# Kernel optimization log

Measured on AMD Instinct MI355X. Metric: run time of the kernel, lower is better.

## Reference

```python
import jax, jax.numpy as jnp
import numpy as np

B = 16384
WIDE_DIM = 256          # 32 wide features * dim 8
DEEP_DIM = 1024         # 64 deep features * embedding_dim 16
SHARED = [2048, 1024, 512]
DOMAIN = [512, 256]
NUM_DOMAINS = 8


def setup_inputs() -> dict:
    key = jax.random.key(0)
    ks = jax.random.split(key, 20)
    s = 0.01  # embedding_init_var-style small init
    inp = {
        "wide_features": jax.random.normal(ks[0], (B, WIDE_DIM), jnp.float32),
        "deep_features": jax.random.normal(ks[1], (B, DEEP_DIM), jnp.float32),
        "domain_ids": jax.random.randint(ks[2], (B,), 0, NUM_DOMAINS, jnp.int64),
        # shared MLP (weights stored [in, out])
        "W1": jax.random.normal(ks[3], (DEEP_DIM, SHARED[0]), jnp.float32) * s,
        "b1": jnp.zeros((SHARED[0],), jnp.float32),
        "W2": jax.random.normal(ks[4], (SHARED[0], SHARED[1]), jnp.float32) * s,
        "b2": jnp.zeros((SHARED[1],), jnp.float32),
        "W3": jax.random.normal(ks[5], (SHARED[1], SHARED[2]), jnp.float32) * s,
        "b3": jnp.zeros((SHARED[2],), jnp.float32),
        # domain-specific MLP
        "Wd1": jax.random.normal(ks[6], (SHARED[2], DOMAIN[0]), jnp.float32) * s,
        "bd1": jnp.zeros((DOMAIN[0],), jnp.float32),
        "Wd2": jax.random.normal(ks[7], (DOMAIN[0], DOMAIN[1]), jnp.float32) * s,
        "bd2": jnp.zeros((DOMAIN[1],), jnp.float32),
        # per-domain output heads: Linear(DOMAIN[-1], 1) per domain
        "Wh": jax.random.normal(ks[8], (NUM_DOMAINS, DOMAIN[1]), jnp.float32) * s,
        "bh": jnp.zeros((NUM_DOMAINS,), jnp.float32),
    }
    return inp


def reference(wide_features, deep_features, domain_ids,
              W1, b1, W2, b2, W3, b3, Wd1, bd1, Wd2, bd2, Wh, bh):
    # wide part: sum embedding output to a scalar logit per sample [B, 1]
    wide = jnp.sum(wide_features, axis=1, keepdims=True)
    # shared deep MLP
    h = jax.nn.relu(deep_features @ W1 + b1)
    h = jax.nn.relu(h @ W2 + b2)
    shared = jax.nn.relu(h @ W3 + b3)          # [B, 512]
    # domain-specific tower (shared across domains)
    d = jax.nn.relu(shared @ Wd1 + bd1)
    d = jax.nn.relu(d @ Wd2 + bd2)             # [B, 256]
    # per-sample domain head routing: gather head weights, fused dot
    w = Wh[domain_ids]                          # [B, 256]
    head = jnp.sum(d * w, axis=1, keepdims=True) + bh[domain_ids][:, None]  # [B, 1]
    out = jax.nn.sigmoid(wide + head)
    return (out, shared, d)
```

## Files before the change

### kernel.cpp

```cpp
#include <hip/hip_runtime.h>
#include <hip/hip_bf16.h>


typedef __attribute__((ext_vector_type(8))) short short8;
typedef __attribute__((ext_vector_type(4))) float f32x4;

static __device__ __forceinline__ unsigned short f2bf_bits(float x) {
  __hip_bfloat16 h = __float2bfloat16(x);
  return __builtin_bit_cast(unsigned short, h);
}
static __device__ __forceinline__ float bf_bits2f(unsigned short u) {
  __hip_bfloat16 h = __builtin_bit_cast(__hip_bfloat16, u);
  return __bfloat162float(h);
}

static __device__ __forceinline__ void gload16(const void* g, void* l) {
  __builtin_amdgcn_global_load_lds(
      (const __attribute__((address_space(1))) void*)g,
      (__attribute__((address_space(3))) void*)l, 16, 0, 0);
}

static __device__ __forceinline__ unsigned lds_u32(const void* p) {
  return (unsigned)(uintptr_t)(const __attribute__((address_space(3))) void*)p;
}

static __device__ __forceinline__ short8 dsr(unsigned addr) {
  short8 r;
  asm volatile("ds_read_b128 %0, %1" : "=v"(r) : "v"(addr));
  return r;
}

#define MFMA16(a, b, c) __builtin_amdgcn_mfma_f32_16x16x32_bf16((a), (b), (c), 0, 0, 0)
#define SB0() __builtin_amdgcn_sched_barrier(0)
#define PRIO(x) __builtin_amdgcn_s_setprio(x)
#define BAR() __builtin_amdgcn_s_barrier()
#define MEMFENCE() asm volatile("" ::: "memory")

__global__ void transpose_convert(const float* __restrict__ W,
                                  __hip_bfloat16* __restrict__ Wt,
                                  int K, int N) {
  __shared__ float tile[64][65];
  const int k0 = blockIdx.y * 64;
  const int n0 = blockIdx.x * 64;
  const int t  = threadIdx.x;
  const int tn = t & 63;
  const int t4 = t >> 6;
#pragma unroll
  for (int p = 0; p < 16; ++p) {
    int kl = p * 4 + t4;
    tile[kl][tn] = W[(size_t)(k0 + kl) * N + (n0 + tn)];
  }
  __syncthreads();
#pragma unroll
  for (int p = 0; p < 16; ++p) {
    int nl = p * 4 + t4;
    Wt[(size_t)(n0 + nl) * K + (k0 + tn)] = __float2bfloat16(tile[tn][nl]);
  }
}

__global__ void f32_to_bf16(const float* __restrict__ in,
                            unsigned short* __restrict__ out, int n8) {
  int i = blockIdx.x * blockDim.x + threadIdx.x;
  if (i >= n8) return;
  const f32x4* p = (const f32x4*)in + (size_t)i * 2;
  f32x4 a = p[0], b = p[1];
  short8 o;
  o[0] = (short)f2bf_bits(a[0]); o[1] = (short)f2bf_bits(a[1]);
  o[2] = (short)f2bf_bits(a[2]); o[3] = (short)f2bf_bits(a[3]);
  o[4] = (short)f2bf_bits(b[0]); o[5] = (short)f2bf_bits(b[1]);
  o[6] = (short)f2bf_bits(b[2]); o[7] = (short)f2bf_bits(b[3]);
  *(short8*)(out + (size_t)i * 8) = o;
}

__global__ __launch_bounds__(512, 2) void gemm_2c(
    const __hip_bfloat16* __restrict__ A,
    const __hip_bfloat16* __restrict__ Bt,
    const float* __restrict__ bias,
    __hip_bfloat16* __restrict__ Cb,
    float* __restrict__ Cf,
    int N, int K, int nbx) {
  __shared__ char lds[131072];

  const int tid  = threadIdx.x;
  const int lane = tid & 63;
  const int wid  = tid >> 6;
  const int wm   = wid >> 2;
  const int wn   = wid & 3;

  const int nwg = gridDim.x;
  const int cpx = nwg >> 3;
  const int id  = blockIdx.x;
  const int swz = (id & 7) * cpx + (id >> 3);
  const int bm  = (swz / nbx) * 256;
  const int bn  = (swz % nbx) * 256;

  const int ln15 = lane & 15;
  const unsigned cswz = (unsigned)((((lane >> 4) ^ (lane & 7)) << 4));

  const unsigned aoff = (unsigned)((wm * 128 + ln15) * 128) + cswz;
  const unsigned boff = 32768u + (unsigned)((wn * 64 + ln15) * 128) + cswz;

  const int nt = K >> 6;

  const __hip_bfloat16* baseA = A  + (size_t)(bm + (tid >> 3)) * K +
                                ((tid & 7) ^ ((tid >> 3) & 7)) * 8;
  const __hip_bfloat16* baseB = Bt + (size_t)(bn + (tid >> 3)) * K +
                                ((tid & 7) ^ ((tid >> 3) & 7)) * 8;
  const unsigned ldst0 = (unsigned)(wid * 1024);

  auto stage = [&](int kt, int half, int isB) {
    const __hip_bfloat16* base = isB ? baseB : baseA;
    char* dst = lds + ((kt & 1) * 65536) + (isB ? 32768 : 0) + half * 16384;
#pragma unroll
    for (int q = 0; q < 2; ++q) {
      gload16(base + (size_t)((half * 128 + q * 64) * K + kt * 64),
              dst + q * 8192 + ldst0);
    }
  };

  auto LD = [&](unsigned off) -> short8 {
    return *(const short8*)&lds[off];
  };

  f32x4 acc[8][4] = {};
  short8 aLo[4][2], aHi[4][2], b0v[2][2], b1v[2][2];

  stage(0, 0, 1); stage(0, 0, 0); stage(0, 1, 1); stage(0, 1, 0);
  if (nt > 1) {
    stage(1, 0, 1); stage(1, 0, 0);
    asm volatile("s_waitcnt vmcnt(4)");
  } else {
    asm volatile("s_waitcnt vmcnt(0)");
  }
  BAR();
  MEMFENCE();
#pragma unroll
  for (int mi = 0; mi < 4; ++mi)
#pragma unroll
    for (int kk = 0; kk < 2; ++kk)
      aLo[mi][kk] = LD((aoff + (unsigned)(mi * 2048)) ^ (unsigned)(kk << 6));
#pragma unroll
  for (int nj = 0; nj < 2; ++nj)
#pragma unroll
    for (int kk = 0; kk < 2; ++kk)
      b0v[nj][kk] = LD((boff + (unsigned)(nj * 2048)) ^ (unsigned)(kk << 6));

  for (int t = 0; t < nt; ++t) {
    const unsigned po = (unsigned)(t & 1) * 65536u;
    const unsigned pn = po ^ 65536u;

#pragma unroll
    for (int nj = 0; nj < 2; ++nj)
#pragma unroll
      for (int kk = 0; kk < 2; ++kk)
        b1v[nj][kk] = LD((po + boff + (unsigned)((nj + 2) * 2048)) ^ (unsigned)(kk << 6));
    if (t + 1 < nt) stage(t + 1, 1, 1);
    PRIO(1);
#pragma unroll
    for (int kk = 0; kk < 2; ++kk)
#pragma unroll
      for (int mi = 0; mi < 4; ++mi)
#pragma unroll
        for (int nj = 0; nj < 2; ++nj)
          acc[mi][nj] = MFMA16(aLo[mi][kk], b0v[nj][kk], acc[mi][nj]);
    PRIO(0);

#pragma unroll
    for (int mi = 0; mi < 4; ++mi)
#pragma unroll
      for (int kk = 0; kk < 2; ++kk)
        aHi[mi][kk] = LD((po + aoff + (unsigned)((mi + 4) * 2048)) ^ (unsigned)(kk << 6));
    if (t + 1 < nt) stage(t + 1, 1, 0);
    PRIO(1);
#pragma unroll
    for (int kk = 0; kk < 2; ++kk)
#pragma unroll
      for (int mi = 0; mi < 4; ++mi)
#pragma unroll
        for (int nj = 0; nj < 2; ++nj)
          acc[mi][nj + 2] = MFMA16(aLo[mi][kk], b1v[nj][kk], acc[mi][nj + 2]);
    PRIO(0);
    BAR();
    MEMFENCE();

    PRIO(1);
#pragma unroll
    for (int kk = 0; kk < 2; ++kk)
#pragma unroll
      for (int mi = 0; mi < 4; ++mi)
#pragma unroll
        for (int nj = 0; nj < 2; ++nj)
          acc[mi + 4][nj] = MFMA16(aHi[mi][kk], b0v[nj][kk], acc[mi + 4][nj]);
    PRIO(0);
    if (t + 2 < nt) stage(t + 2, 0, 1);
    if (t + 1 < nt) {
      if (t + 2 < nt) asm volatile("s_waitcnt vmcnt(2)");
      else            asm volatile("s_waitcnt vmcnt(0)");
      BAR();
      MEMFENCE();
    }

    if (t + 1 < nt) {
#pragma unroll
      for (int mi = 0; mi < 4; ++mi)
#pragma unroll
        for (int kk = 0; kk < 2; ++kk)
          aLo[mi][kk] = LD((pn + aoff + (unsigned)(mi * 2048)) ^ (unsigned)(kk << 6));
#pragma unroll
      for (int nj = 0; nj < 2; ++nj)
#pragma unroll
        for (int kk = 0; kk < 2; ++kk)
          b0v[nj][kk] = LD((pn + boff + (unsigned)(nj * 2048)) ^ (unsigned)(kk << 6));
    }
    PRIO(1);
#pragma unroll
    for (int kk = 0; kk < 2; ++kk)
#pragma unroll
      for (int mi = 0; mi < 4; ++mi)
#pragma unroll
        for (int nj = 0; nj < 2; ++nj)
          acc[mi + 4][nj + 2] = MFMA16(aHi[mi][kk], b1v[nj][kk], acc[mi + 4][nj + 2]);
    PRIO(0);
    if (t + 2 < nt) stage(t + 2, 0, 0);
  }

  float biasv[4];
#pragma unroll
  for (int nj = 0; nj < 4; ++nj)
    biasv[nj] = bias[bn + wn * 64 + nj * 16 + ln15];

#pragma unroll
  for (int mi = 0; mi < 8; ++mi) {
    int row0 = bm + wm * 128 + mi * 16 + (lane >> 4) * 4;
#pragma unroll
    for (int nj = 0; nj < 4; ++nj) {
      int col = bn + wn * 64 + nj * 16 + ln15;
#pragma unroll
      for (int r = 0; r < 4; ++r) {
        float v = acc[mi][nj][r] + biasv[nj];
        v = v > 0.f ? v : 0.f;
        size_t idx = (size_t)(row0 + r) * N + col;
        Cb[idx] = __float2bfloat16(v);
        if (Cf) Cf[idx] = v;
      }
    }
  }
}

__global__ __launch_bounds__(512, 2) void gemm_128(
    const __hip_bfloat16* __restrict__ A,
    const __hip_bfloat16* __restrict__ Bt,
    const float* __restrict__ bias,
    __hip_bfloat16* __restrict__ Cb,
    float* __restrict__ Cf,
    int N, int K, int nbx) {
  __shared__ char lds[98304];

  const int tid  = threadIdx.x;
  const int lane = tid & 63;
  const int wid  = tid >> 6;
  const int wm   = wid >> 2;
  const int wn   = wid & 3;

  const int nwg = gridDim.x;
  const int cpx = nwg >> 3;
  const int id  = blockIdx.x;
  const int swz = (id & 7) * cpx + (id >> 3);
  const int bm  = (swz / nbx) * 128;
  const int bn  = (swz % nbx) * 256;

  const int ln15 = lane & 15;
  const unsigned cswz = (unsigned)((((lane >> 4) ^ (lane & 7)) << 4));

  const unsigned lbase = lds_u32(lds);
  const unsigned arow0 = lbase + (unsigned)(wm * 64 + ln15) * 128u + cswz;
  const unsigned brow0 = lbase + 16384u + (unsigned)(wn * 64 + ln15) * 128u + cswz;

  const int nt = K >> 6;

  const int swc = (tid & 7) ^ ((tid >> 3) & 7);
  const __hip_bfloat16* baseA = A  + (size_t)(bm + (tid >> 3)) * K + swc * 8;
  const __hip_bfloat16* baseB = Bt + (size_t)(bn + (tid >> 3)) * K + swc * 8;
  const unsigned ldst0 = (unsigned)(tid * 16);

  auto stageA = [&](int kt, int half) {
    char* dst = lds + ((kt & 1) * 49152) + half * 8192;
    gload16(baseA + (size_t)((half * 64) * K + kt * 64), dst + ldst0);
  };
  auto stageB = [&](int kt, int half) {
    char* dst = lds + ((kt & 1) * 49152) + 16384 + half * 16384;
#pragma unroll
    for (int q = 0; q < 2; ++q) {
      gload16(baseB + (size_t)((half * 128 + q * 64) * K + kt * 64),
              dst + q * 8192 + ldst0);
    }
  };

  f32x4 acc[4][4] = {};
  short8 aLo[2][2], aHi[2][2], b0v[2][2], b1v[2][2];

  stageB(0, 0); stageA(0, 0); stageB(0, 1); stageA(0, 1);
  if (nt > 1) {
    stageB(1, 0); stageA(1, 0);
    asm volatile("s_waitcnt vmcnt(3)");
  } else {
    asm volatile("s_waitcnt vmcnt(0)");
  }
  BAR();
#pragma unroll
  for (int mi = 0; mi < 2; ++mi) {
    unsigned ad = arow0 + (unsigned)(mi * 2048);
    aLo[mi][0] = dsr(ad); aLo[mi][1] = dsr(ad ^ 64u);
  }

  for (int t = 0; t < nt; ++t) {
    const unsigned po = (unsigned)(t & 1) * 49152u;
    const unsigned pn = po ^ 49152u;

    asm volatile("s_waitcnt lgkmcnt(0)");
    SB0();
#pragma unroll
    for (int nj = 0; nj < 2; ++nj) b0v[nj][0] = dsr(brow0 + po + (unsigned)(nj * 2048));
#pragma unroll
    for (int nj = 0; nj < 2; ++nj) b0v[nj][1] = dsr((brow0 + po + (unsigned)(nj * 2048)) ^ 64u);
#pragma unroll
    for (int nj = 0; nj < 2; ++nj) b1v[nj][0] = dsr(brow0 + po + (unsigned)((nj + 2) * 2048));
#pragma unroll
    for (int nj = 0; nj < 2; ++nj) b1v[nj][1] = dsr((brow0 + po + (unsigned)((nj + 2) * 2048)) ^ 64u);
    if (t + 1 < nt) stageB(t + 1, 1);
    asm volatile("s_waitcnt lgkmcnt(6)");
    SB0();
    PRIO(1);
#pragma unroll
    for (int mi = 0; mi < 2; ++mi)
#pragma unroll
      for (int nj = 0; nj < 2; ++nj)
        acc[mi][nj] = MFMA16(aLo[mi][0], b0v[nj][0], acc[mi][nj]);
    asm volatile("s_waitcnt lgkmcnt(4)");
    SB0();
#pragma unroll
    for (int mi = 0; mi < 2; ++mi)
#pragma unroll
      for (int nj = 0; nj < 2; ++nj)
        acc[mi][nj] = MFMA16(aLo[mi][1], b0v[nj][1], acc[mi][nj]);
    PRIO(0);

#pragma unroll
    for (int mi = 0; mi < 2; ++mi) {
      unsigned ad = arow0 + po + (unsigned)((mi + 2) * 2048);
      aHi[mi][0] = dsr(ad); aHi[mi][1] = dsr(ad ^ 64u);
    }
    if (t + 1 < nt) stageA(t + 1, 1);
    asm volatile("s_waitcnt lgkmcnt(4)");
    SB0();
    PRIO(1);
#pragma unroll
    for (int kk = 0; kk < 2; ++kk)
#pragma unroll
      for (int mi = 0; mi < 2; ++mi)
#pragma unroll
        for (int nj = 0; nj < 2; ++nj)
          acc[mi][nj + 2] = MFMA16(aLo[mi][kk], b1v[nj][kk], acc[mi][nj + 2]);
    PRIO(0);
    BAR();

    asm volatile("s_waitcnt lgkmcnt(0)");
    SB0();
    PRIO(1);
#pragma unroll
    for (int kk = 0; kk < 2; ++kk)
#pragma unroll
      for (int mi = 0; mi < 2; ++mi)
#pragma unroll
        for (int nj = 0; nj < 2; ++nj)
          acc[mi + 2][nj] = MFMA16(aHi[mi][kk], b0v[nj][kk], acc[mi + 2][nj]);
    PRIO(0);
    if (t + 2 < nt) stageB(t + 2, 0);
    if (t + 2 < nt)      asm volatile("s_waitcnt vmcnt(2)");
    else if (t + 1 < nt) asm volatile("s_waitcnt vmcnt(0)");
    if (t + 1 < nt) BAR();

    if (t + 1 < nt) {
#pragma unroll
      for (int mi = 0; mi < 2; ++mi) {
        unsigned ad = arow0 + pn + (unsigned)(mi * 2048);
        aLo[mi][0] = dsr(ad); aLo[mi][1] = dsr(ad ^ 64u);
      }
    }
    SB0();
    PRIO(1);
#pragma unroll
    for (int kk = 0; kk < 2; ++kk)
#pragma unroll
      for (int mi = 0; mi < 2; ++mi)
#pragma unroll
        for (int nj = 0; nj < 2; ++nj)
          acc[mi + 2][nj + 2] = MFMA16(aHi[mi][kk], b1v[nj][kk], acc[mi + 2][nj + 2]);
    PRIO(0);
    if (t + 2 < nt) stageA(t + 2, 0);
  }

  float biasv[4];
#pragma unroll
  for (int nj = 0; nj < 4; ++nj)
    biasv[nj] = bias[bn + wn * 64 + nj * 16 + ln15];

#pragma unroll
  for (int mi = 0; mi < 4; ++mi) {
    int row0 = bm + wm * 64 + mi * 16 + (lane >> 4) * 4;
#pragma unroll
    for (int nj = 0; nj < 4; ++nj) {
      int col = bn + wn * 64 + nj * 16 + ln15;
#pragma unroll
      for (int r = 0; r < 4; ++r) {
        float v = acc[mi][nj][r] + biasv[nj];
        v = v > 0.f ? v : 0.f;
        size_t idx = (size_t)(row0 + r) * N + col;
        Cb[idx] = __float2bfloat16(v);
        if (Cf) Cf[idx] = v;
      }
    }
  }
}

__global__ __launch_bounds__(256, 2) void gemm_bt(
    const __hip_bfloat16* __restrict__ A,
    const __hip_bfloat16* __restrict__ Bt,
    const float* __restrict__ bias,
    __hip_bfloat16* __restrict__ Cb,
    float* __restrict__ Cf,
    int N, int K) {
  __shared__ char lds[32768];

  const int tid  = threadIdx.x;
  const int lane = tid & 63;
  const int wid  = tid >> 6;
  const int wm   = wid >> 1;
  const int wn   = wid & 1;
  const int bm   = blockIdx.y * 128;
  const int bn   = blockIdx.x * 128;

  f32x4 acc[4][4] = {};

  const int srow = tid >> 3;
  const int sk   = (tid & 7) * 8;
  const int kTiles = K >> 6;

  for (int kt = 0; kt < kTiles; ++kt) {
    __syncthreads();
    const __hip_bfloat16* ga = A  + (size_t)(bm + srow) * K + kt * 64 + sk;
    const __hip_bfloat16* gb = Bt + (size_t)(bn + srow) * K + kt * 64 + sk;
#pragma unroll
    for (int p = 0; p < 4; ++p) {
      gload16(ga + (size_t)(p * 32) * K, &lds[p * 4096 + wid * 1024]);
      gload16(gb + (size_t)(p * 32) * K, &lds[16384 + p * 4096 + wid * 1024]);
    }
    __syncthreads();

#pragma unroll
    for (int kk = 0; kk < 2; ++kk) {
      short8 avec[4], bvec[4];
#pragma unroll
      for (int i = 0; i < 4; ++i) {
        int row = wm * 64 + i * 16 + (lane & 15);
        avec[i] = *(const short8*)&lds[row * 128 + kk * 64 + (lane >> 4) * 16];
      }
#pragma unroll
      for (int j = 0; j < 4; ++j) {
        int row = wn * 64 + j * 16 + (lane & 15);
        bvec[j] = *(const short8*)&lds[16384 + row * 128 + kk * 64 + (lane >> 4) * 16];
      }
#pragma unroll
      for (int i = 0; i < 4; ++i)
#pragma unroll
        for (int j = 0; j < 4; ++j)
          acc[i][j] = MFMA16(avec[i], bvec[j], acc[i][j]);
    }
  }

  float biasv[4];
#pragma unroll
  for (int j = 0; j < 4; ++j)
    biasv[j] = bias[bn + wn * 64 + j * 16 + (lane & 15)];

#pragma unroll
  for (int i = 0; i < 4; ++i) {
    int row0 = bm + wm * 64 + i * 16 + (lane >> 4) * 4;
#pragma unroll
    for (int j = 0; j < 4; ++j) {
      int col = bn + wn * 64 + j * 16 + (lane & 15);
#pragma unroll
      for (int r = 0; r < 4; ++r) {
        float v = acc[i][j][r] + biasv[j];
        v = v > 0.f ? v : 0.f;
        size_t idx = (size_t)(row0 + r) * N + col;
        Cb[idx] = __float2bfloat16(v);
        if (Cf) Cf[idx] = v;
      }
    }
  }
}

__global__ __launch_bounds__(256) void head_kernel(
    const float* __restrict__ wide,
    const __hip_bfloat16* __restrict__ D,
    const int* __restrict__ dom,
    const float* __restrict__ Wh,
    const float* __restrict__ bh,
    float* __restrict__ out, int B) {
  const int wid  = threadIdx.x >> 6;
  const int lane = threadIdx.x & 63;
  const int row  = blockIdx.x * 4 + wid;
  if (row >= B) return;
  const int dm = dom[row];

  f32x4 wv = ((const f32x4*)(wide + (size_t)row * 256))[lane];
  float tot = wv[0] + wv[1] + wv[2] + wv[3];

  const unsigned short* drow = (const unsigned short*)(D + (size_t)row * 256);
  ushort4 dv = ((const ushort4*)drow)[lane];
  f32x4 hv = ((const f32x4*)(Wh + (size_t)dm * 256))[lane];
  tot += bf_bits2f(dv.x) * hv[0] + bf_bits2f(dv.y) * hv[1] +
         bf_bits2f(dv.z) * hv[2] + bf_bits2f(dv.w) * hv[3];

#pragma unroll
  for (int off = 32; off > 0; off >>= 1) tot += __shfl_xor(tot, off);

  if (lane == 0) {
    float x = tot + bh[dm];
    out[row] = 1.f / (1.f + __expf(-x));
  }
}

extern "C" void kernel_launch(void* const* d_in, const int* in_sizes, int n_in,
                              void* d_out, int out_size, void* d_ws, size_t ws_size,
                              hipStream_t stream) {
  const float* wide = (const float*)d_in[0];
  const float* deep = (const float*)d_in[1];
  const int*   dom  = (const int*)d_in[2];
  const float* W1  = (const float*)d_in[3];
  const float* b1  = (const float*)d_in[4];
  const float* W2  = (const float*)d_in[5];
  const float* b2  = (const float*)d_in[6];
  const float* W3  = (const float*)d_in[7];
  const float* b3  = (const float*)d_in[8];
  const float* Wd1 = (const float*)d_in[9];
  const float* bd1 = (const float*)d_in[10];
  const float* Wd2 = (const float*)d_in[11];
  const float* bd2 = (const float*)d_in[12];
  const float* Wh  = (const float*)d_in[13];
  const float* bh  = (const float*)d_in[14];
  float* out = (float*)d_out;

  const int B = 16384;
  char* ws = (char*)d_ws;
  __hip_bfloat16* buf0 = (__hip_bfloat16*)ws;
  __hip_bfloat16* buf1 = (__hip_bfloat16*)(ws + 33554432ull);
  __hip_bfloat16* W1t  = (__hip_bfloat16*)(ws + 100663296ull);
  __hip_bfloat16* W2t  = W1t + 2048 * 1024;
  __hip_bfloat16* W3t  = W2t + 1024 * 2048;
  __hip_bfloat16* Wd1t = W3t + 512 * 1024;
  __hip_bfloat16* Wd2t = Wd1t + 512 * 512;

  transpose_convert<<<dim3(2048 / 64, 1024 / 64), 256, 0, stream>>>(W1, W1t, 1024, 2048);
  transpose_convert<<<dim3(1024 / 64, 2048 / 64), 256, 0, stream>>>(W2, W2t, 2048, 1024);
  transpose_convert<<<dim3(512 / 64, 1024 / 64), 256, 0, stream>>>(W3, W3t, 1024, 512);
  transpose_convert<<<dim3(512 / 64, 512 / 64), 256, 0, stream>>>(Wd1, Wd1t, 512, 512);
  transpose_convert<<<dim3(256 / 64, 512 / 64), 256, 0, stream>>>(Wd2, Wd2t, 512, 256);

  {
    int n8 = B * 1024 / 8;
    f32_to_bf16<<<(n8 + 255) / 256, 256, 0, stream>>>(deep, (unsigned short*)buf0, n8);
  }

  float* shared_out = out + B;
  float* d_out_f    = out + B + (size_t)B * 512;

  gemm_2c<<<dim3((2048 / 256) * (B / 256)), 512, 0, stream>>>(
      buf0, W1t, b1, buf1, nullptr, 2048, 1024, 2048 / 256);
  gemm_2c<<<dim3((1024 / 256) * (B / 256)), 512, 0, stream>>>(
      buf1, W2t, b2, buf0, nullptr, 1024, 2048, 1024 / 256);
  gemm_128<<<dim3((B / 128) * (512 / 256)), 512, 0, stream>>>(
      buf0, W3t, b3, buf1, shared_out, 512, 1024, 512 / 256);
  gemm_128<<<dim3((B / 128) * (512 / 256)), 512, 0, stream>>>(
      buf1, Wd1t, bd1, buf0, nullptr, 512, 512, 512 / 256);
  gemm_bt<<<dim3(256 / 128, B / 128), 256, 0, stream>>>(buf0, Wd2t, bd2, buf1, d_out_f, 256, 512);

  head_kernel<<<B / 4, 256, 0, stream>>>(wide, buf1, dom, Wh, bh, out, B);
}
```

Measured before the change: 224.3 us.

## Fuse prep kernels, fuse tower GEMMs and head, restage gemm_2c loads

```diff
diff --git a/kernel.cpp b/kernel.cpp
--- a/kernel.cpp
+++ b/kernel.cpp
@@ -18,16 +18,6 @@
   __builtin_amdgcn_global_load_lds(
       (const __attribute__((address_space(1))) void*)g,
       (__attribute__((address_space(3))) void*)l, 16, 0, 0);
-}
-
-static __device__ __forceinline__ unsigned lds_u32(const void* p) {
-  return (unsigned)(uintptr_t)(const __attribute__((address_space(3))) void*)p;
-}
-
-static __device__ __forceinline__ short8 dsr(unsigned addr) {
-  short8 r;
-  asm volatile("ds_read_b128 %0, %1" : "=v"(r) : "v"(addr));
-  return r;
 }
 
 #define MFMA16(a, b, c) __builtin_amdgcn_mfma_f32_16x16x32_bf16((a), (b), (c), 0, 0, 0)
@@ -36,12 +26,37 @@
 #define BAR() __builtin_amdgcn_s_barrier()
 #define MEMFENCE() asm volatile("" ::: "memory")
 
-__global__ void transpose_convert(const float* __restrict__ W,
-                                  __hip_bfloat16* __restrict__ Wt,
-                                  int K, int N) {
+__global__ __launch_bounds__(256) void prep(
+    const float* __restrict__ deep, unsigned short* __restrict__ deepb,
+    const float* __restrict__ W1, __hip_bfloat16* __restrict__ W1t,
+    const float* __restrict__ W2, __hip_bfloat16* __restrict__ W2t,
+    const float* __restrict__ W3, __hip_bfloat16* __restrict__ W3t,
+    const float* __restrict__ Wd1, __hip_bfloat16* __restrict__ Wd1t,
+    const float* __restrict__ Wd2, __hip_bfloat16* __restrict__ Wd2t) {
   __shared__ float tile[64][65];
-  const int k0 = blockIdx.y * 64;
-  const int n0 = blockIdx.x * 64;
+  int blk = blockIdx.x;
+  if (blk < 8192) {
+    int i = blk * 256 + threadIdx.x;
+    const f32x4* p = (const f32x4*)deep + (size_t)i * 2;
+    f32x4 a = p[0], b = p[1];
+    short8 o;
+    o[0] = (short)f2bf_bits(a[0]); o[1] = (short)f2bf_bits(a[1]);
+    o[2] = (short)f2bf_bits(a[2]); o[3] = (short)f2bf_bits(a[3]);
+    o[4] = (short)f2bf_bits(b[0]); o[5] = (short)f2bf_bits(b[1]);
+    o[6] = (short)f2bf_bits(b[2]); o[7] = (short)f2bf_bits(b[3]);
+    *(short8*)(deepb + (size_t)i * 8) = o;
+    return;
+  }
+  blk -= 8192;
+  const float* W; __hip_bfloat16* Wt; int K, N;
+  if (blk < 512)       {             W = W1;  Wt = W1t;  K = 1024; N = 2048; }
+  else if (blk < 1024) { blk -= 512;  W = W2;  Wt = W2t;  K = 2048; N = 1024; }
+  else if (blk < 1152) { blk -= 1024; W = W3;  Wt = W3t;  K = 1024; N = 512; }
+  else if (blk < 1216) { blk -= 1152; W = Wd1; Wt = Wd1t; K = 512;  N = 512; }
+  else                 { blk -= 1216; W = Wd2; Wt = Wd2t; K = 512;  N = 256; }
+  const int ntx = N >> 6;
+  const int k0 = (blk / ntx) * 64;
+  const int n0 = (blk % ntx) * 64;
   const int t  = threadIdx.x;
   const int tn = t & 63;
   const int t4 = t >> 6;
@@ -56,20 +71,6 @@
     int nl = p * 4 + t4;
     Wt[(size_t)(n0 + nl) * K + (k0 + tn)] = __float2bfloat16(tile[tn][nl]);
   }
-}
-
-__global__ void f32_to_bf16(const float* __restrict__ in,
-                            unsigned short* __restrict__ out, int n8) {
-  int i = blockIdx.x * blockDim.x + threadIdx.x;
-  if (i >= n8) return;
-  const f32x4* p = (const f32x4*)in + (size_t)i * 2;
-  f32x4 a = p[0], b = p[1];
-  short8 o;
-  o[0] = (short)f2bf_bits(a[0]); o[1] = (short)f2bf_bits(a[1]);
-  o[2] = (short)f2bf_bits(a[2]); o[3] = (short)f2bf_bits(a[3]);
-  o[4] = (short)f2bf_bits(b[0]); o[5] = (short)f2bf_bits(b[1]);
-  o[6] = (short)f2bf_bits(b[2]); o[7] = (short)f2bf_bits(b[3]);
-  *(short8*)(out + (size_t)i * 8) = o;
 }
 
 __global__ __launch_bounds__(512, 2) void gemm_2c(
@@ -95,10 +96,10 @@
   const int bn  = (swz % nbx) * 256;
 
   const int ln15 = lane & 15;
-  const unsigned cswz = (unsigned)((((lane >> 4) ^ (lane & 7)) << 4));
-
-  const unsigned aoff = (unsigned)((wm * 128 + ln15) * 128) + cswz;
-  const unsigned boff = 32768u + (unsigned)((wn * 64 + ln15) * 128) + cswz;
+  const unsigned aoff = (unsigned)((wm * 128 + ln15) * 128) +
+                        (unsigned)((((lane >> 4) ^ (lane & 7)) << 4));
+  const unsigned boff = 32768u + (unsigned)((wn * 64 + ln15) * 128) +
+                        (unsigned)((((lane >> 4) ^ (lane & 7)) << 4));
 
   const int nt = K >> 6;
 
@@ -125,10 +126,10 @@
   f32x4 acc[8][4] = {};
   short8 aLo[4][2], aHi[4][2], b0v[2][2], b1v[2][2];
 
-  stage(0, 0, 1); stage(0, 0, 0); stage(0, 1, 1); stage(0, 1, 0);
+  stage(0, 0, 1); stage(0, 1, 1); stage(0, 0, 0); stage(0, 1, 0);
   if (nt > 1) {
-    stage(1, 0, 1); stage(1, 0, 0);
-    asm volatile("s_waitcnt vmcnt(4)");
+    stage(1, 0, 1); stage(1, 1, 1); stage(1, 0, 0); stage(1, 1, 0);
+    asm volatile("s_waitcnt vmcnt(8)");
   } else {
     asm volatile("s_waitcnt vmcnt(0)");
   }
@@ -154,7 +155,6 @@
 #pragma unroll
       for (int kk = 0; kk < 2; ++kk)
         b1v[nj][kk] = LD((po + boff + (unsigned)((nj + 2) * 2048)) ^ (unsigned)(kk << 6));
-    if (t + 1 < nt) stage(t + 1, 1, 1);
     PRIO(1);
 #pragma unroll
     for (int kk = 0; kk < 2; ++kk)
@@ -170,7 +170,6 @@
 #pragma unroll
       for (int kk = 0; kk < 2; ++kk)
         aHi[mi][kk] = LD((po + aoff + (unsigned)((mi + 4) * 2048)) ^ (unsigned)(kk << 6));
-    if (t + 1 < nt) stage(t + 1, 1, 0);
     PRIO(1);
 #pragma unroll
     for (int kk = 0; kk < 2; ++kk)
@@ -192,9 +191,9 @@
         for (int nj = 0; nj < 2; ++nj)
           acc[mi + 4][nj] = MFMA16(aHi[mi][kk], b0v[nj][kk], acc[mi + 4][nj]);
     PRIO(0);
-    if (t + 2 < nt) stage(t + 2, 0, 1);
+    if (t + 2 < nt) { stage(t + 2, 0, 1); stage(t + 2, 1, 1); }
     if (t + 1 < nt) {
-      if (t + 2 < nt) asm volatile("s_waitcnt vmcnt(2)");
+      if (t + 2 < nt) asm volatile("s_waitcnt vmcnt(4)");
       else            asm volatile("s_waitcnt vmcnt(0)");
       BAR();
       MEMFENCE();
@@ -221,7 +220,7 @@
         for (int nj = 0; nj < 2; ++nj)
           acc[mi + 4][nj + 2] = MFMA16(aHi[mi][kk], b1v[nj][kk], acc[mi + 4][nj + 2]);
     PRIO(0);
-    if (t + 2 < nt) stage(t + 2, 0, 0);
+    if (t + 2 < nt) { stage(t + 2, 0, 0); stage(t + 2, 1, 0); }
   }
 
   float biasv[4];
@@ -247,288 +246,257 @@
   }
 }
 
-__global__ __launch_bounds__(512, 2) void gemm_128(
-    const __hip_bfloat16* __restrict__ A,
-    const __hip_bfloat16* __restrict__ Bt,
-    const float* __restrict__ bias,
-    __hip_bfloat16* __restrict__ Cb,
-    float* __restrict__ Cf,
-    int N, int K, int nbx) {
-  __shared__ char lds[98304];
-
+__global__ __launch_bounds__(512, 2) void tower(
+    const __hip_bfloat16* __restrict__ H2,
+    const __hip_bfloat16* __restrict__ W3t, const float* __restrict__ b3,
+    const __hip_bfloat16* __restrict__ Wd1t, const float* __restrict__ bd1,
+    const __hip_bfloat16* __restrict__ Wd2t, const float* __restrict__ bd2,
+    float* __restrict__ Sf, float* __restrict__ Df,
+    const float* __restrict__ wide, const int* __restrict__ dom,
+    const float* __restrict__ Wh, const float* __restrict__ bh,
+    float* __restrict__ outp) {
+  __shared__ char lds[139264];
   const int tid  = threadIdx.x;
   const int lane = tid & 63;
   const int wid  = tid >> 6;
-  const int wm   = wid >> 2;
-  const int wn   = wid & 3;
-
-  const int nwg = gridDim.x;
-  const int cpx = nwg >> 3;
+  const int ln15 = lane & 15;
+  const int kq   = lane >> 4;
+
   const int id  = blockIdx.x;
-  const int swz = (id & 7) * cpx + (id >> 3);
-  const int bm  = (swz / nbx) * 128;
-  const int bn  = (swz % nbx) * 256;
-
-  const int ln15 = lane & 15;
-  const unsigned cswz = (unsigned)((((lane >> 4) ^ (lane & 7)) << 4));
-
-  const unsigned lbase = lds_u32(lds);
-  const unsigned arow0 = lbase + (unsigned)(wm * 64 + ln15) * 128u + cswz;
-  const unsigned brow0 = lbase + 16384u + (unsigned)(wn * 64 + ln15) * 128u + cswz;
-
-  const int nt = K >> 6;
-
-  const int swc = (tid & 7) ^ ((tid >> 3) & 7);
-  const __hip_bfloat16* baseA = A  + (size_t)(bm + (tid >> 3)) * K + swc * 8;
-  const __hip_bfloat16* baseB = Bt + (size_t)(bn + (tid >> 3)) * K + swc * 8;
-  const unsigned ldst0 = (unsigned)(tid * 16);
-
-  auto stageA = [&](int kt, int half) {
-    char* dst = lds + ((kt & 1) * 49152) + half * 8192;
-    gload16(baseA + (size_t)((half * 64) * K + kt * 64), dst + ldst0);
+  const int swz = (id & 7) * 32 + (id >> 3);
+  const int bm  = swz * 64;
+
+  const unsigned csel = (unsigned)(((unsigned)kq ^ (unsigned)((ln15 >> 1) & 3)) << 4);
+  const int sc   = (tid & 3) ^ ((tid >> 3) & 3);
+  const int srow = tid >> 2;
+
+  auto LD = [&](unsigned off) -> short8 { return *(const short8*)&lds[off]; };
+
+  auto stage3 = [&](int kt) {
+    int half = kt & 1;
+#pragma unroll
+    for (int q = 0; q < 4; ++q)
+      gload16(W3t + (size_t)(q * 128 + srow) * 1024 + kt * 32 + sc * 8,
+              lds + 73728 + half * 32768 + q * 8192 + tid * 16);
+    if (tid < 256)
+      gload16(H2 + (size_t)(bm + srow) * 1024 + kt * 32 + sc * 8,
+              lds + 65536 + half * 4096 + tid * 16);
   };
-  auto stageB = [&](int kt, int half) {
-    char* dst = lds + ((kt & 1) * 49152) + 16384 + half * 16384;
-#pragma unroll
-    for (int q = 0; q < 2; ++q) {
-      gload16(baseB + (size_t)((half * 128 + q * 64) * K + kt * 64),
-              dst + q * 8192 + ldst0);
-    }
+
+  f32x4 acc3[4][4] = {};
+  stage3(0);
+  for (int t = 0; t < 32; ++t) {
+    if (t + 1 < 32) {
+      stage3(t + 1);
+      if (wid < 4) asm volatile("s_waitcnt vmcnt(5)");
+      else         asm volatile("s_waitcnt vmcnt(4)");
+    } else {
+      asm volatile("s_waitcnt vmcnt(0)");
+    }
+    BAR(); MEMFENCE();
+    const unsigned pa = 65536u + (unsigned)((t & 1) * 4096);
+    const unsigned pb = 73728u + (unsigned)((t & 1) * 32768);
+    short8 aF[4], bF[4];
+#pragma unroll
+    for (int mi = 0; mi < 4; ++mi)
+      aF[mi] = LD(pa + (unsigned)((mi * 16 + ln15) * 64) + csel);
+#pragma unroll
+    for (int nj = 0; nj < 4; ++nj)
+      bF[nj] = LD(pb + (unsigned)((wid * 64 + nj * 16 + ln15) * 64) + csel);
+    PRIO(1);
+#pragma unroll
+    for (int mi = 0; mi < 4; ++mi)
+#pragma unroll
+      for (int nj = 0; nj < 4; ++nj)
+        acc3[mi][nj] = MFMA16(aF[mi], bF[nj], acc3[mi][nj]);
+    PRIO(0);
+    BAR(); MEMFENCE();
+  }
+
+  {
+    float bv[4];
+#pragma unroll
+    for (int nj = 0; nj < 4; ++nj) bv[nj] = b3[wid * 64 + nj * 16 + ln15];
+#pragma unroll
+    for (int mi = 0; mi < 4; ++mi) {
+      int lrow = mi * 16 + kq * 4;
+#pragma unroll
+      for (int nj = 0; nj < 4; ++nj) {
+        int col = wid * 64 + nj * 16 + ln15;
+#pragma unroll
+        for (int r = 0; r < 4; ++r) {
+          float v = acc3[mi][nj][r] + bv[nj];
+          v = v > 0.f ? v : 0.f;
+          Sf[(size_t)(bm + lrow + r) * 512 + col] = v;
+          int rr = lrow + r;
+          *(unsigned short*)&lds[rr * 1024 + (((col >> 3) ^ (rr & 7)) << 4) +
+                                 (col & 7) * 2] = f2bf_bits(v);
+        }
+      }
+    }
+  }
+
+  auto stage4 = [&](int kt) {
+    int half = kt & 1;
+#pragma unroll
+    for (int q = 0; q < 4; ++q)
+      gload16(Wd1t + (size_t)(q * 128 + srow) * 512 + kt * 32 + sc * 8,
+              lds + 73728 + half * 32768 + q * 8192 + tid * 16);
   };
-
-  f32x4 acc[4][4] = {};
-  short8 aLo[2][2], aHi[2][2], b0v[2][2], b1v[2][2];
-
-  stageB(0, 0); stageA(0, 0); stageB(0, 1); stageA(0, 1);
-  if (nt > 1) {
-    stageB(1, 0); stageA(1, 0);
-    asm volatile("s_waitcnt vmcnt(3)");
-  } else {
-    asm volatile("s_waitcnt vmcnt(0)");
-  }
-  BAR();
-#pragma unroll
-  for (int mi = 0; mi < 2; ++mi) {
-    unsigned ad = arow0 + (unsigned)(mi * 2048);
-    aLo[mi][0] = dsr(ad); aLo[mi][1] = dsr(ad ^ 64u);
-  }
-
-  for (int t = 0; t < nt; ++t) {
-    const unsigned po = (unsigned)(t & 1) * 49152u;
-    const unsigned pn = po ^ 49152u;
-
-    asm volatile("s_waitcnt lgkmcnt(0)");
-    SB0();
-#pragma unroll
-    for (int nj = 0; nj < 2; ++nj) b0v[nj][0] = dsr(brow0 + po + (unsigned)(nj * 2048));
-#pragma unroll
-    for (int nj = 0; nj < 2; ++nj) b0v[nj][1] = dsr((brow0 + po + (unsigned)(nj * 2048)) ^ 64u);
-#pragma unroll
-    for (int nj = 0; nj < 2; ++nj) b1v[nj][0] = dsr(brow0 + po + (unsigned)((nj + 2) * 2048));
-#pragma unroll
-    for (int nj = 0; nj < 2; ++nj) b1v[nj][1] = dsr((brow0 + po + (unsigned)((nj + 2) * 2048)) ^ 64u);
-    if (t + 1 < nt) stageB(t + 1, 1);
-    asm volatile("s_waitcnt lgkmcnt(6)");
-    SB0();
-    PRIO(1);
-#pragma unroll
-    for (int mi = 0; mi < 2; ++mi)
+  stage4(0);
+  asm volatile("s_waitcnt lgkmcnt(0)");
+  BAR(); MEMFENCE();
+
+  f32x4 acc4[4][4] = {};
+  for (int t = 0; t < 16; ++t) {
+    if (t + 1 < 16) { stage4(t + 1); asm volatile("s_waitcnt vmcnt(4)"); }
+    else            { asm volatile("s_waitcnt vmcnt(0)"); }
+    BAR(); MEMFENCE();
+    const unsigned pb = 73728u + (unsigned)((t & 1) * 32768);
+    short8 aF[4], bF[4];
+#pragma unroll
+    for (int mi = 0; mi < 4; ++mi) {
+      int rr = mi * 16 + ln15;
+      aF[mi] = LD((unsigned)(rr * 1024) +
+                  (unsigned)((((t * 4 + kq) ^ (rr & 7)) << 4)));
+    }
+#pragma unroll
+    for (int nj = 0; nj < 4; ++nj)
+      bF[nj] = LD(pb + (unsigned)((wid * 64 + nj * 16 + ln15) * 64) + csel);
+    PRIO(1);
+#pragma unroll
+    for (int mi = 0; mi < 4; ++mi)
+#pragma unroll
+      for (int nj = 0; nj < 4; ++nj)
+        acc4[mi][nj] = MFMA16(aF[mi], bF[nj], acc4[mi][nj]);
+    PRIO(0);
+    BAR(); MEMFENCE();
+  }
+
+  {
+    float bv[4];
+#pragma unroll
+    for (int nj = 0; nj < 4; ++nj) bv[nj] = bd1[wid * 64 + nj * 16 + ln15];
+#pragma unroll
+    for (int mi = 0; mi < 4; ++mi) {
+      int lrow = mi * 16 + kq * 4;
+#pragma unroll
+      for (int nj = 0; nj < 4; ++nj) {
+        int col = wid * 64 + nj * 16 + ln15;
+#pragma unroll
+        for (int r = 0; r < 4; ++r) {
+          float v = acc4[mi][nj][r] + bv[nj];
+          v = v > 0.f ? v : 0.f;
+          int rr = lrow + r;
+          *(unsigned short*)&lds[rr * 1024 + (((col >> 3) ^ (rr & 7)) << 4) +
+                                 (col & 7) * 2] = f2bf_bits(v);
+        }
+      }
+    }
+  }
+
+  auto stage5 = [&](int kt) {
+    int half = kt & 1;
+#pragma unroll
+    for (int q = 0; q < 2; ++q)
+      gload16(Wd2t + (size_t)(q * 128 + srow) * 512 + kt * 32 + sc * 8,
+              lds + 73728 + half * 16384 + q * 8192 + tid * 16);
+  };
+  stage5(0);
+  asm volatile("s_waitcnt lgkmcnt(0)");
+  BAR(); MEMFENCE();
+
+  f32x4 acc5[4][2] = {};
+  for (int t = 0; t < 16; ++t) {
+    if (t + 1 < 16) { stage5(t + 1); asm volatile("s_waitcnt vmcnt(2)"); }
+    else            { asm volatile("s_waitcnt vmcnt(0)"); }
+    BAR(); MEMFENCE();
+    const unsigned pb = 73728u + (unsigned)((t & 1) * 16384);
+    short8 aF[4], bF[2];
+#pragma unroll
+    for (int mi = 0; mi < 4; ++mi) {
+      int rr = mi * 16 + ln15;
+      aF[mi] = LD((unsigned)(rr * 1024) +
+                  (unsigned)((((t * 4 + kq) ^ (rr & 7)) << 4)));
+    }
+#pragma unroll
+    for (int nj = 0; nj < 2; ++nj)
+      bF[nj] = LD(pb + (unsigned)((wid * 32 + nj * 16 + ln15) * 64) + csel);
+    PRIO(1);
+#pragma unroll
+    for (int mi = 0; mi < 4; ++mi)
 #pragma unroll
       for (int nj = 0; nj < 2; ++nj)
-        acc[mi][nj] = MFMA16(aLo[mi][0], b0v[nj][0], acc[mi][nj]);
-    asm volatile("s_waitcnt lgkmcnt(4)");
-    SB0();
-#pragma unroll
-    for (int mi = 0; mi < 2; ++mi)
-#pragma unroll
-      for (int nj = 0; nj < 2; ++nj)
-        acc[mi][nj] = MFMA16(aLo[mi][1], b0v[nj][1], acc[mi][nj]);
-    PRIO(0);
-
-#pragma unroll
-    for (int mi = 0; mi < 2; ++mi) {
-      unsigned ad = arow0 + po + (unsigned)((mi + 2) * 2048);
-      aHi[mi][0] = dsr(ad); aHi[mi][1] = dsr(ad ^ 64u);
-    }
-    if (t + 1 < nt) stageA(t + 1, 1);
-    asm volatile("s_waitcnt lgkmcnt(4)");
-    SB0();
-    PRIO(1);
-#pragma unroll
-    for (int kk = 0; kk < 2; ++kk)
-#pragma unroll
-      for (int mi = 0; mi < 2; ++mi)
-#pragma unroll
-        for (int nj = 0; nj < 2; ++nj)
-          acc[mi][nj + 2] = MFMA16(aLo[mi][kk], b1v[nj][kk], acc[mi][nj + 2]);
-    PRIO(0);
-    BAR();
-
-    asm volatile("s_waitcnt lgkmcnt(0)");
-    SB0();
-    PRIO(1);
-#pragma unroll
-    for (int kk = 0; kk < 2; ++kk)
-#pragma unroll
-      for (int mi = 0; mi < 2; ++mi)
-#pragma unroll
-        for (int nj = 0; nj < 2; ++nj)
-          acc[mi + 2][nj] = MFMA16(aHi[mi][kk], b0v[nj][kk], acc[mi + 2][nj]);
-    PRIO(0);
-    if (t + 2 < nt) stageB(t + 2, 0);
-    if (t + 2 < nt)      asm volatile("s_waitcnt vmcnt(2)");
-    else if (t + 1 < nt) asm volatile("s_waitcnt vmcnt(0)");
-    if (t + 1 < nt) BAR();
-
-    if (t + 1 < nt) {
-#pragma unroll
-      for (int mi = 0; mi < 2; ++mi) {
-        unsigned ad = arow0 + pn + (unsigned)(mi * 2048);
-        aLo[mi][0] = dsr(ad); aLo[mi][1] = dsr(ad ^ 64u);
+        acc5[mi][nj] = MFMA16(aF[mi], bF[nj], acc5[mi][nj]);
+    PRIO(0);
+    BAR(); MEMFENCE();
+  }
+
+  unsigned short* ldsD = (unsigned short*)(lds + 65536);
+  {
+    float bv[2];
+#pragma unroll
+    for (int nj = 0; nj < 2; ++nj) bv[nj] = bd2[wid * 32 + nj * 16 + ln15];
+#pragma unroll
+    for (int mi = 0; mi < 4; ++mi) {
+      int lrow = mi * 16 + kq * 4;
+#pragma unroll
+      for (int nj = 0; nj < 2; ++nj) {
+        int col = wid * 32 + nj * 16 + ln15;
+#pragma unroll
+        for (int r = 0; r < 4; ++r) {
+          float v = acc5[mi][nj][r] + bv[nj];
+          v = v > 0.f ? v : 0.f;
+          Df[(size_t)(bm + lrow + r) * 256 + col] = v;
+          ldsD[(lrow + r) * 264 + col] = f2bf_bits(v);
+        }
       }
     }
-    SB0();
-    PRIO(1);
-#pragma unroll
-    for (int kk = 0; kk < 2; ++kk)
-#pragma unroll
-      for (int mi = 0; mi < 2; ++mi)
-#pragma unroll
-        for (int nj = 0; nj < 2; ++nj)
-          acc[mi + 2][nj + 2] = MFMA16(aHi[mi][kk], b1v[nj][kk], acc[mi + 2][nj + 2]);
-    PRIO(0);
-    if (t + 2 < nt) stageA(t + 2, 0);
-  }
-
-  float biasv[4];
-#pragma unroll
-  for (int nj = 0; nj < 4; ++nj)
-    biasv[nj] = bias[bn + wn * 64 + nj * 16 + ln15];
-
-#pragma unroll
-  for (int mi = 0; mi < 4; ++mi) {
-    int row0 = bm + wm * 64 + mi * 16 + (lane >> 4) * 4;
-#pragma unroll
-    for (int nj = 0; nj < 4; ++nj) {
-      int col = bn + wn * 64 + nj * 16 + ln15;
-#pragma unroll
-      for (int r = 0; r < 4; ++r) {
-        float v = acc[mi][nj][r] + biasv[nj];
-        v = v > 0.f ? v : 0.f;
-        size_t idx = (size_t)(row0 + r) * N + col;
-        Cb[idx] = __float2bfloat16(v);
-        if (Cf) Cf[idx] = v;
-      }
-    }
-  }
-}
-
-__global__ __launch_bounds__(256, 2) void gemm_bt(
-    const __hip_bfloat16* __restrict__ A,
-    const __hip_bfloat16* __restrict__ Bt,
-    const float* __restrict__ bias,
-    __hip_bfloat16* __restrict__ Cb,
-    float* __restrict__ Cf,
-    int N, int K) {
-  __shared__ char lds[32768];
-
-  const int tid  = threadIdx.x;
-  const int lane = tid & 63;
-  const int wid  = tid >> 6;
-  const int wm   = wid >> 1;
-  const int wn   = wid & 1;
-  const int bm   = blockIdx.y * 128;
-  const int bn   = blockIdx.x * 128;
-
-  f32x4 acc[4][4] = {};
-
-  const int srow = tid >> 3;
-  const int sk   = (tid & 7) * 8;
-  const int kTiles = K >> 6;
-
-  for (int kt = 0; kt < kTiles; ++kt) {
-    __syncthreads();
-    const __hip_bfloat16* ga = A  + (size_t)(bm + srow) * K + kt * 64 + sk;
-    const __hip_bfloat16* gb = Bt + (size_t)(bn + srow) * K + kt * 64 + sk;
-#pragma unroll
-    for (int p = 0; p < 4; ++p) {
-      gload16(ga + (size_t)(p * 32) * K, &lds[p * 4096 + wid * 1024]);
-      gload16(gb + (size_t)(p * 32) * K, &lds[16384 + p * 4096 + wid * 1024]);
-    }
-    __syncthreads();
-
-#pragma unroll
-    for (int kk = 0; kk < 2; ++kk) {
-      short8 avec[4], bvec[4];
-#pragma unroll
-      for (int i = 0; i < 4; ++i) {
-        int row = wm * 64 + i * 16 + (lane & 15);
-        avec[i] = *(const short8*)&lds[row * 128 + kk * 64 + (lane >> 4) * 16];
-      }
-#pragma unroll
-      for (int j = 0; j < 4; ++j) {
-        int row = wn * 64 + j * 16 + (lane & 15);
-        bvec[j] = *(const short8*)&lds[16384 + row * 128 + kk * 64 + (lane >> 4) * 16];
-      }
-#pragma unroll
-      for (int i = 0; i < 4; ++i)
-#pragma unroll
-        for (int j = 0; j < 4; ++j)
-          acc[i][j] = MFMA16(avec[i], bvec[j], acc[i][j]);
-    }
-  }
-
-  float biasv[4];
-#pragma unroll
-  for (int j = 0; j < 4; ++j)
-    biasv[j] = bias[bn + wn * 64 + j * 16 + (lane & 15)];
-
-#pragma unroll
-  for (int i = 0; i < 4; ++i) {
-    int row0 = bm + wm * 64 + i * 16 + (lane >> 4) * 4;
+  }
+  asm volatile("s_waitcnt lgkmcnt(0)");
+  BAR(); MEMFENCE();
+
+  const int hrow = tid >> 3;
+  const int he   = tid & 7;
+  float s = 0.f;
+  {
+    const f32x4* wp = (const f32x4*)(wide + (size_t)(bm + hrow) * 256 + he * 32);
+#pragma unroll
+    for (int j = 0; j < 8; ++j) {
+      f32x4 w = wp[j];
+      s += w[0] + w[1] + w[2] + w[3];
+    }
+  }
+  const int dm = dom[bm + hrow];
+  {
+    const f32x4* hp = (const f32x4*)(Wh + (size_t)dm * 256 + he * 32);
+    const short8* dp = (const short8*)(ldsD + hrow * 264 + he * 32);
 #pragma unroll
     for (int j = 0; j < 4; ++j) {
-      int col = bn + wn * 64 + j * 16 + (lane & 15);
-#pragma unroll
-      for (int r = 0; r < 4; ++r) {
-        float v = acc[i][j][r] + biasv[j];
-        v = v > 0.f ? v : 0.f;
-        size_t idx = (size_t)(row0 + r) * N + col;
-        Cb[idx] = __float2bfloat16(v);
-        if (Cf) Cf[idx] = v;
-      }
-    }
-  }
-}
-
-__global__ __launch_bounds__(256) void head_kernel(
-    const float* __restrict__ wide,
-    const __hip_bfloat16* __restrict__ D,
-    const int* __restrict__ dom,
-    const float* __restrict__ Wh,
-    const float* __restrict__ bh,
-    float* __restrict__ out, int B) {
-  const int wid  = threadIdx.x >> 6;
-  const int lane = threadIdx.x & 63;
-  const int row  = blockIdx.x * 4 + wid;
-  if (row >= B) return;
-  const int dm = dom[row];
-
-  f32x4 wv = ((const f32x4*)(wide + (size_t)row * 256))[lane];
-  float tot = wv[0] + wv[1] + wv[2] + wv[3];
-
-  const unsigned short* drow = (const unsigned short*)(D + (size_t)row * 256);
-  ushort4 dv = ((const ushort4*)drow)[lane];
-  f32x4 hv = ((const f32x4*)(Wh + (size_t)dm * 256))[lane];
-  tot += bf_bits2f(dv.x) * hv[0] + bf_bits2f(dv.y) * hv[1] +
-         bf_bits2f(dv.z) * hv[2] + bf_bits2f(dv.w) * hv[3];
-
-#pragma unroll
-  for (int off = 32; off > 0; off >>= 1) tot += __shfl_xor(tot, off);
-
-  if (lane == 0) {
-    float x = tot + bh[dm];
-    out[row] = 1.f / (1.f + __expf(-x));
+      short8 d8 = dp[j];
+      f32x4 h0 = hp[2 * j], h1 = hp[2 * j + 1];
+      s += bf_bits2f((unsigned short)d8[0]) * h0[0] +
+           bf_bits2f((unsigned short)d8[1]) * h0[1] +
+           bf_bits2f((unsigned short)d8[2]) * h0[2] +
+           bf_bits2f((unsigned short)d8[3]) * h0[3] +
+           bf_bits2f((unsigned short)d8[4]) * h1[0] +
+           bf_bits2f((unsigned short)d8[5]) * h1[1] +
+           bf_bits2f((unsigned short)d8[6]) * h1[2] +
+           bf_bits2f((unsigned short)d8[7]) * h1[3];
+    }
+  }
+  float* ldsH = (float*)(lds + 100352);
+  ldsH[hrow * 8 + he] = s;
+  asm volatile("s_waitcnt lgkmcnt(0)");
+  BAR(); MEMFENCE();
+
+  if (tid < 64) {
+    float v = 0.f;
+#pragma unroll
+    for (int j = 0; j < 8; ++j) v += ldsH[tid * 8 + j];
+    int dmr = dom[bm + tid];
+    float x = v + bh[dmr];
+    outp[bm + tid] = 1.f / (1.f + __expf(-x));
   }
 }
 
@@ -562,16 +530,8 @@
   __hip_bfloat16* Wd1t = W3t + 512 * 1024;
   __hip_bfloat16* Wd2t = Wd1t + 512 * 512;
 
-  transpose_convert<<<dim3(2048 / 64, 1024 / 64), 256, 0, stream>>>(W1, W1t, 1024, 2048);
-  transpose_convert<<<dim3(1024 / 64, 2048 / 64), 256, 0, stream>>>(W2, W2t, 2048, 1024);
-  transpose_convert<<<dim3(512 / 64, 1024 / 64), 256, 0, stream>>>(W3, W3t, 1024, 512);
-  transpose_convert<<<dim3(512 / 64, 512 / 64), 256, 0, stream>>>(Wd1, Wd1t, 512, 512);
-  transpose_convert<<<dim3(256 / 64, 512 / 64), 256, 0, stream>>>(Wd2, Wd2t, 512, 256);
-
-  {
-    int n8 = B * 1024 / 8;
-    f32_to_bf16<<<(n8 + 255) / 256, 256, 0, stream>>>(deep, (unsigned short*)buf0, n8);
-  }
+  prep<<<dim3(8192 + 1248), 256, 0, stream>>>(
+      deep, (unsigned short*)buf0, W1, W1t, W2, W2t, W3, W3t, Wd1, Wd1t, Wd2, Wd2t);
 
   float* shared_out = out + B;
   float* d_out_f    = out + B + (size_t)B * 512;
@@ -580,11 +540,7 @@
       buf0, W1t, b1, buf1, nullptr, 2048, 1024, 2048 / 256);
   gemm_2c<<<dim3((1024 / 256) * (B / 256)), 512, 0, stream>>>(
       buf1, W2t, b2, buf0, nullptr, 1024, 2048, 1024 / 256);
-  gemm_128<<<dim3((B / 128) * (512 / 256)), 512, 0, stream>>>(
-      buf0, W3t, b3, buf1, shared_out, 512, 1024, 512 / 256);
-  gemm_128<<<dim3((B / 128) * (512 / 256)), 512, 0, stream>>>(
-      buf1, Wd1t, bd1, buf0, nullptr, 512, 512, 512 / 256);
-  gemm_bt<<<dim3(256 / 128, B / 128), 256, 0, stream>>>(buf0, Wd2t, bd2, buf1, d_out_f, 256, 512);
-
-  head_kernel<<<B / 4, 256, 0, stream>>>(wide, buf1, dom, Wh, bh, out, B);
-}
+  tower<<<dim3(256), 512, 0, stream>>>(
+      buf0, W3t, b3, Wd1t, bd1, Wd2t, bd2,
+      shared_out, d_out_f, wide, dom, Wh, bh, out);
+}
```

New measurement: 200.7 us. 1.12x faster.
